# Kernel tuning notes

Measured on AMD Instinct MI355X. Metric: run time of the kernel, lower is better.

Reference implementation:

```python
import jax, jax.numpy as jnp
import numpy as np

N, E, ND, ED, H, OUT, L, VC = 10000, 160000, 8, 4, 128, 256, 6, 6
HEADS, C = 4, 128  # GATConv: out_channels=128 per head, concat=False -> mean over heads


def _ln(x, g, b, eps=1e-5):
    m = x.mean(-1, keepdims=True)
    v = ((x - m) ** 2).mean(-1, keepdims=True)
    return (x - m) * jax.lax.rsqrt(v + eps) * g + b


def _gat_layer(h, src, dst, e_attr, lw, a_src, a_dst, lew, a_edge, bias):
    # h: [N,H]; e_attr: [Etot,H]; PyG GATConv(heads=4, concat=False, edge_dim=H)
    xh = (h @ lw).reshape(N, HEADS, C)                 # [N,4,128]
    eh = (e_attr @ lew).reshape(-1, HEADS, C)          # [Etot,4,128]
    al_s = jnp.einsum('nhc,hc->nh', xh, a_src)
    al_d = jnp.einsum('nhc,hc->nh', xh, a_dst)
    al_e = jnp.einsum('ehc,hc->eh', eh, a_edge)
    alpha = jax.nn.leaky_relu(al_s[src] + al_d[dst] + al_e, 0.2)  # [Etot,4]
    amax = jax.ops.segment_max(alpha, dst, num_segments=N)
    ex = jnp.exp(alpha - amax[dst])
    den = jax.ops.segment_sum(ex, dst, num_segments=N)
    w = ex / (den[dst] + 1e-16)
    out = jax.ops.segment_sum(xh[src] * w[..., None], dst, num_segments=N)  # [N,4,128]
    return out.mean(axis=1) + bias


def setup_inputs() -> dict:
    key = jax.random.key(0)
    ks = jax.random.split(key, 32)
    s = 0.05
    d = {
        'x': jax.random.normal(ks[0], (N, ND), jnp.float32),
        'edge_index': jax.random.randint(ks[1], (2, E), 0, N),
        'edge_attr': jax.random.uniform(ks[2], (E, ED), jnp.float32),
        'vnf_context': jax.random.normal(ks[3], (1, VC), jnp.float32),
        # node embedding
        'node_w': jax.random.normal(ks[4], (ND, H)) * s, 'node_b': jnp.zeros((H,)),
        # EdgeAttentionLayer
        'ea_proj_w': jax.random.normal(ks[5], (ED, H)) * s, 'ea_proj_b': jnp.zeros((H,)),
        'vnf_w': jax.random.normal(ks[6], (VC, H)) * s, 'vnf_b': jnp.zeros((H,)),
        'att1_w': jax.random.normal(ks[7], (2 * H, H)) * s, 'att1_b': jnp.zeros((H,)),
        'att2_w': jax.random.normal(ks[8], (H, H // 2)) * s, 'att2_b': jnp.zeros((H // 2,)),
        'att3_w': jax.random.normal(ks[9], (H // 2, 1)) * s, 'att3_b': jnp.zeros((1,)),
        # per-layer GATConv params (stacked over L layers)
        'gat_lin_w': jax.random.normal(ks[10], (L, H, HEADS * C)) * s,
        'gat_att_src': jax.random.normal(ks[11], (L, HEADS, C)) * s,
        'gat_att_dst': jax.random.normal(ks[12], (L, HEADS, C)) * s,
        'gat_lin_edge_w': jax.random.normal(ks[13], (L, H, HEADS * C)) * s,
        'gat_att_edge': jax.random.normal(ks[14], (L, HEADS, C)) * s,
        'gat_bias': jnp.zeros((L, C)),
        'ln_scale': jnp.ones((L, H)), 'ln_bias': jnp.zeros((L, H)),
        # output projection
        'out_w': jax.random.normal(ks[15], (H, OUT)) * s, 'out_b': jnp.zeros((OUT,)),
    }
    return d


def reference(x, edge_index, edge_attr, vnf_context, node_w, node_b, ea_proj_w, ea_proj_b,
              vnf_w, vnf_b, att1_w, att1_b, att2_w, att2_b, att3_w, att3_b,
              gat_lin_w, gat_att_src, gat_att_dst, gat_lin_edge_w, gat_att_edge, gat_bias,
              ln_scale, ln_bias, out_w, out_b):
    src, dst = edge_index[0], edge_index[1]
    h = x @ node_w + node_b                                   # [N,128]
    # EdgeAttentionLayer (eval mode, no network_state)
    ef = edge_attr @ ea_proj_w + ea_proj_b                    # [E,128]
    vnf = vnf_context @ vnf_w + vnf_b                         # [1,128]
    comb = jnp.concatenate([ef, jnp.broadcast_to(vnf, (E, H))], axis=-1)
    a = jax.nn.relu(comb @ att1_w + att1_b)
    a = jax.nn.relu(a @ att2_w + att2_b)
    e_gate = jax.nn.sigmoid(a @ att3_w + att3_b)              # [E,1]
    w_edge = ef * e_gate                                      # [E,128]
    # GATConv default add_self_loops=True, fill_value='mean'
    loop = jnp.arange(N)
    src2 = jnp.concatenate([src, loop])
    dst2 = jnp.concatenate([dst, loop])
    e2 = jnp.concatenate([w_edge, jnp.broadcast_to(w_edge.mean(0, keepdims=True), (N, H))], axis=0)
    for l in range(L):
        hc = _gat_layer(h, src2, dst2, e2, gat_lin_w[l], gat_att_src[l], gat_att_dst[l],
                        gat_lin_edge_w[l], gat_att_edge[l], gat_bias[l])
        h = _ln(h + jax.nn.relu(hc), ln_scale[l], ln_bias[l])
    return h @ out_w + out_b                                  # [N,256]
```

## Files before the change

### kernel.cpp

```cpp
#include <hip/hip_runtime.h>
#include <hip/hip_bf16.h>
#include <math.h>

#define Nn 10000
#define Ee 160000
#define ET 170000
#define LL 6

typedef short v8s __attribute__((ext_vector_type(8)));
typedef float v4f __attribute__((ext_vector_type(4)));

__device__ __forceinline__ unsigned short f2bf(float v) {
    unsigned int b = __float_as_uint(v);
    b += 0x7fffu + ((b >> 16) & 1u);
    return (unsigned short)(b >> 16);
}
__device__ __forceinline__ float bflo(unsigned int u) { return __uint_as_float(u << 16); }
__device__ __forceinline__ float bfhi(unsigned int u) { return __uint_as_float(u & 0xffff0000u); }

__global__ __launch_bounds__(256) void k_first(
    const float* __restrict__ x, const float* __restrict__ nw,
    const float* __restrict__ nb, float* __restrict__ h, unsigned short* __restrict__ hb,
    const int* __restrict__ ei, int* __restrict__ hist,
    const float* __restrict__ glw, const float* __restrict__ gas,
    const float* __restrict__ gad, const float* __restrict__ glew,
    const float* __restrict__ gae, float* __restrict__ Bs,
    float* __restrict__ Bd, float* __restrict__ Be) {
    int b = blockIdx.x, t = threadIdx.x;
    if (b < 5000) {
        int idx = b * 256 + t;
        int n = idx >> 7, c = idx & 127;
        const float* xr = x + (size_t)n * 8;
        float acc = nb[c];
#pragma unroll
        for (int k = 0; k < 8; k++) acc += xr[k] * nw[k * 128 + c];
        h[idx] = acc;
        hb[idx] = f2bf(acc);
        return;
    }
    if (b < 5665) {
        int i = (b - 5000) * 256 + t;
        if (i < ET) {
            int d = (i < Ee) ? ei[Ee + i] : (i - Ee);
            atomicAdd(&hist[d], 1);
        }
        return;
    }
    {
        int idx = (b - 5665) * 256 + t;
        if (idx >= LL * 128 * 4) return;
        int hh = idx & 3, k = (idx >> 2) & 127, l = idx >> 9;
        const float* lwp = glw  + (size_t)l * 65536 + k * 512 + hh * 128;
        const float* lep = glew + (size_t)l * 65536 + k * 512 + hh * 128;
        const float* sp = gas + l * 512 + hh * 128;
        const float* dp = gad + l * 512 + hh * 128;
        const float* ep = gae + l * 512 + hh * 128;
        float s1 = 0, s2 = 0, s3 = 0;
        for (int c = 0; c < 128; c++) {
            float lv = lwp[c];
            s1 += lv * sp[c];
            s2 += lv * dp[c];
            s3 += lep[c] * ep[c];
        }
        Bs[idx] = s1; Bd[idx] = s2; Be[idx] = s3;
    }
}

__global__ __launch_bounds__(256) void k_setup(
    const float* __restrict__ glw, unsigned short* __restrict__ WsumT,
    const float* __restrict__ a2w, unsigned short* __restrict__ w2bf,
    const float* __restrict__ vnfc, const float* __restrict__ vw,
    const float* __restrict__ vb, const float* __restrict__ eab,
    const float* __restrict__ a1w, const float* __restrict__ a1b,
    const float* __restrict__ eaw, float* __restrict__ E1,
    const float* __restrict__ Be, float* __restrict__ PB, float* __restrict__ cB) {
    __shared__ float vr[128];
    __shared__ float sM1[512];
    __shared__ float sd1[128];
    int b = blockIdx.x, t = threadIdx.x;
    if (b < 1536) {
        int idx = b * 256 + t;
        int kk = idx & 511;
        int c = (idx >> 9) & 127;
        int l = idx >> 16;
        float v = 0.25f * glw[(size_t)l * 65536 + (size_t)(kk & 127) * 512 + (kk >> 7) * 128 + c];
        WsumT[(size_t)l * 65536 + (size_t)c * 512 + kk] = f2bf(v);
        return;
    }
    if (b < 1568) {
        int idx = (b - 1536) * 256 + t;
        int j = idx & 7, lane = (idx >> 3) & 63, nt = (idx >> 9) & 3, ks = idx >> 11;
        int k = ks * 32 + ((lane >> 4) << 3) + j;
        int n = nt * 16 + (lane & 15);
        w2bf[idx] = f2bf(a2w[k * 64 + n]);
        return;
    }
    if (b == 1568) {
        if (t < 128) {
            float a = vb[t];
#pragma unroll
            for (int k = 0; k < 6; k++) a += vnfc[k] * vw[k * 128 + t];
            vr[t] = a;
        }
        __syncthreads();
        if (t < 128) {
            float a = a1b[t];
            for (int k = 0; k < 128; k++) a += eab[k] * a1w[k * 128 + t];
            for (int k = 0; k < 128; k++) a += vr[k] * a1w[(128 + k) * 128 + t];
            sd1[t] = a;
        }
#pragma unroll
        for (int rr = 0; rr < 2; rr++) {
            int id = rr * 256 + t;
            int r = id >> 7, j = id & 127;
            float a = 0.f;
            for (int k = 0; k < 128; k++) a += eaw[r * 128 + k] * a1w[k * 128 + j];
            sM1[id] = a;
        }
        __syncthreads();
        if (t < 128) {
            E1[t * 8 + 0] = sM1[t];
            E1[t * 8 + 1] = sM1[128 + t];
            E1[t * 8 + 2] = sM1[256 + t];
            E1[t * 8 + 3] = sM1[384 + t];
            E1[t * 8 + 4] = sd1[t];
            E1[t * 8 + 5] = 0.f; E1[t * 8 + 6] = 0.f; E1[t * 8 + 7] = 0.f;
        }
        return;
    }
    {
        if (t >= 24) return;
        int l = t >> 2, hh = t & 3;
        const float* bp = Be + l * 512 + hh;
        float s0 = 0, s1 = 0, s2 = 0, s3 = 0, sc = 0;
        for (int k = 0; k < 128; k++) {
            float bv = bp[k * 4];
            s0 += eaw[0 * 128 + k] * bv;
            s1 += eaw[1 * 128 + k] * bv;
            s2 += eaw[2 * 128 + k] * bv;
            s3 += eaw[3 * 128 + k] * bv;
            sc += eab[k] * bv;
        }
        PB[0 * 24 + t] = s0; PB[1 * 24 + t] = s1;
        PB[2 * 24 + t] = s2; PB[3 * 24 + t] = s3;
        cB[t] = sc;
    }
}

__global__ __launch_bounds__(1024) void k_scan(const int* __restrict__ hist,
                                               int* __restrict__ seg, int* __restrict__ pos) {
    __shared__ int wsums[16];
    __shared__ int carry_s;
    int t = threadIdx.x;
    int lane = t & 63, wid = t >> 6;
    if (t == 0) { carry_s = 0; seg[0] = 0; }
    __syncthreads();
    for (int base = 0; base < Nn; base += 1024) {
        int idx = base + t;
        int v = (idx < Nn) ? hist[idx] : 0;
        int sc = v;
#pragma unroll
        for (int d = 1; d < 64; d <<= 1) {
            int up = __shfl_up(sc, d);
            if (lane >= d) sc += up;
        }
        if (lane == 63) wsums[wid] = sc;
        __syncthreads();
        if (wid == 0) {
            int wv = (lane < 16) ? wsums[lane] : 0;
            int wsc = wv;
#pragma unroll
            for (int d = 1; d < 16; d <<= 1) {
                int up = __shfl_up(wsc, d);
                if (lane >= d) wsc += up;
            }
            if (lane < 16) wsums[lane] = wsc - wv;
        }
        __syncthreads();
        int carry = carry_s;
        int inc = sc + wsums[wid] + carry;
        if (idx < Nn) { seg[idx + 1] = inc; pos[idx] = inc - v; }
        __syncthreads();
        if (t == 1023) carry_s = inc;
        __syncthreads();
    }
}

__global__ void k_scatter(const int* __restrict__ ei, int* __restrict__ pos,
                          int* __restrict__ srcv, int* __restrict__ inv,
                          int* __restrict__ loopslot) {
    int i = blockIdx.x * 256 + threadIdx.x;
    if (i >= ET) return;
    int s, d;
    if (i < Ee) { s = ei[i]; d = ei[Ee + i]; } else { s = d = i - Ee; }
    int idx = atomicAdd(&pos[d], 1);
    srcv[idx] = s;
    if (i < Ee) inv[i] = idx;
    else        loopslot[i - Ee] = idx;
}

__global__ __launch_bounds__(256, 2) void k_edge(
    const float* __restrict__ ea, const float* __restrict__ E1,
    const unsigned short* __restrict__ w2bf,
    const float* __restrict__ a2b, const float* __restrict__ a3w,
    const float* __restrict__ a3b,
    const float* __restrict__ PB, const float* __restrict__ cB,
    const int* __restrict__ inv,
    float* __restrict__ aleT, float* __restrict__ gsum) {
    __shared__ float4 sM[128];
    __shared__ float sD[128];
    __shared__ float4 sevs[256];
    __shared__ float gsh[256];
    __shared__ float sgsum[5];
    int t = threadIdx.x;
    int lane = t & 63;
    int wid = t >> 6;
    int c = lane & 15, q = lane >> 4;
    int eb0 = blockIdx.x * 256;

    sevs[t] = *(const float4*)(ea + (size_t)(eb0 + t) * 4);
    if (t < 128) {
        int slot = t ^ ((t >> 3) & 3);
        sM[slot] = *(const float4*)(E1 + t * 8);
        sD[t] = E1[t * 8 + 4];
    }
    if (t < 5) sgsum[t] = 0.f;
    __syncthreads();

    float4 ev4[4];
#pragma unroll
    for (int mt = 0; mt < 4; mt++) ev4[mt] = sevs[(wid * 4 + mt) * 16 + c];

    v8s av[4][4];
#pragma unroll
    for (int ks = 0; ks < 4; ks++) {
        float4 mr[8]; float dr[8];
#pragma unroll
        for (int j = 0; j < 8; j++) {
            int k = ks * 32 + q * 8 + j;
            mr[j] = sM[k ^ q];
            dr[j] = sD[k];
        }
#pragma unroll
        for (int mt = 0; mt < 4; mt++) {
            float4 ev = ev4[mt];
            v8s a;
#pragma unroll
            for (int j = 0; j < 8; j++) {
                float xv = fmaxf(dr[j] + ev.x * mr[j].x + ev.y * mr[j].y
                                       + ev.z * mr[j].z + ev.w * mr[j].w, 0.f);
                a[j] = (short)f2bf(xv);
            }
            av[mt][ks] = a;
        }
    }

    v4f acc[4][4];
#pragma unroll
    for (int nt = 0; nt < 4; nt++) {
        float bb = a2b[nt * 16 + c];
#pragma unroll
        for (int mt = 0; mt < 4; mt++) acc[mt][nt] = (v4f){bb, bb, bb, bb};
    }
#pragma unroll
    for (int nt = 0; nt < 4; nt++) {
#pragma unroll
        for (int ks = 0; ks < 4; ks++) {
            v8s bfr = *(const v8s*)(w2bf + ((size_t)(ks * 4 + nt) * 64 + lane) * 8);
#pragma unroll
            for (int mt = 0; mt < 4; mt++)
                acc[mt][nt] = __builtin_amdgcn_mfma_f32_16x16x32_bf16(av[mt][ks], bfr, acc[mt][nt], 0, 0, 0);
        }
    }

    float a3r[4];
#pragma unroll
    for (int nt = 0; nt < 4; nt++) a3r[nt] = a3w[nt * 16 + c];
    float a3b0 = a3b[0];
#pragma unroll
    for (int mt = 0; mt < 4; mt++) {
#pragma unroll
        for (int r = 0; r < 4; r++) {
            float s = 0.f;
#pragma unroll
            for (int nt = 0; nt < 4; nt++) s += fmaxf(acc[mt][nt][r], 0.f) * a3r[nt];
            s += __shfl_xor(s, 1); s += __shfl_xor(s, 2);
            s += __shfl_xor(s, 4); s += __shfl_xor(s, 8);
            if (c == 0) gsh[(wid * 4 + mt) * 16 + q * 4 + r] = 1.f / (1.f + __expf(-(s + a3b0)));
        }
    }
    __syncthreads();

    float g = gsh[t];
    float4 evv = sevs[t];
    float v0 = g, v1 = g * evv.x, v2 = g * evv.y, v3 = g * evv.z, v4 = g * evv.w;
#pragma unroll
    for (int d = 32; d > 0; d >>= 1) {
        v0 += __shfl_down(v0, d); v1 += __shfl_down(v1, d); v2 += __shfl_down(v2, d);
        v3 += __shfl_down(v3, d); v4 += __shfl_down(v4, d);
    }
    if (lane == 0) {
        atomicAdd(&sgsum[0], v0); atomicAdd(&sgsum[1], v1); atomicAdd(&sgsum[2], v2);
        atomicAdd(&sgsum[3], v3); atomicAdd(&sgsum[4], v4);
    }
    __syncthreads();
    if (t < 5) atomicAdd(&gsum[t], sgsum[t]);
    int slot = inv[eb0 + t];
#pragma unroll
    for (int i4 = 0; i4 < 6; i4++) {
        float4 cc = *(const float4*)(cB + i4 * 4);
        float4 p0 = *(const float4*)(PB + 0 * 24 + i4 * 4);
        float4 p1 = *(const float4*)(PB + 1 * 24 + i4 * 4);
        float4 p2 = *(const float4*)(PB + 2 * 24 + i4 * 4);
        float4 p3 = *(const float4*)(PB + 3 * 24 + i4 * 4);
        float4 o;
        o.x = g * (cc.x + evv.x * p0.x + evv.y * p1.x + evv.z * p2.x + evv.w * p3.x);
        o.y = g * (cc.y + evv.x * p0.y + evv.y * p1.y + evv.z * p2.y + evv.w * p3.y);
        o.z = g * (cc.z + evv.x * p0.z + evv.y * p1.z + evv.z * p2.z + evv.w * p3.z);
        o.w = g * (cc.w + evv.x * p0.w + evv.y * p1.w + evv.z * p2.w + evv.w * p3.w);
        *(float4*)(aleT + (size_t)i4 * ET * 4 + (size_t)slot * 4) = o;
    }
}

__global__ __launch_bounds__(256) void k_abfill(
    const float* __restrict__ h, const float* __restrict__ Bs_l,
    const float* __restrict__ Bd_l, float* __restrict__ als, float* __restrict__ ald,
    const int* __restrict__ loopslot, const float* __restrict__ gsum,
    const float* __restrict__ PB, const float* __restrict__ cB,
    float* __restrict__ aleT) {
    int b = blockIdx.x, t = threadIdx.x;
    if (b < 313) {
        int idx = b * 256 + t;
        if (idx >= Nn * 8) return;
        int n = idx >> 3, slot = idx & 7;
        const float* B = (slot < 4) ? Bs_l : Bd_l;
        int hh = slot & 3;
        const float4* hr = (const float4*)(h + (size_t)n * 128);
        float s = 0.f;
#pragma unroll 8
        for (int kb = 0; kb < 32; kb++) {
            float4 hv = hr[kb];
            s += hv.x * B[(4 * kb + 0) * 4 + hh] + hv.y * B[(4 * kb + 1) * 4 + hh]
               + hv.z * B[(4 * kb + 2) * 4 + hh] + hv.w * B[(4 * kb + 3) * 4 + hh];
        }
        if (slot < 4) als[n * 4 + hh] = s;
        else          ald[n * 4 + hh] = s;
        return;
    }
    {
        int idx = (b - 313) * 256 + t;
        if (idx >= LL * Nn) return;
        int l = idx / Nn;
        int j = idx - l * Nn;
        int slot = loopslot[j];
        float g0 = gsum[0], g1 = gsum[1], g2 = gsum[2], g3 = gsum[3], g4 = gsum[4];
        float4 cc = *(const float4*)(cB + l * 4);
        float4 p0 = *(const float4*)(PB + 0 * 24 + l * 4);
        float4 p1 = *(const float4*)(PB + 1 * 24 + l * 4);
        float4 p2 = *(const float4*)(PB + 2 * 24 + l * 4);
        float4 p3 = *(const float4*)(PB + 3 * 24 + l * 4);
        float4 o;
        o.x = (g0 * cc.x + g1 * p0.x + g2 * p1.x + g3 * p2.x + g4 * p3.x) * (1.0f / Ee);
        o.y = (g0 * cc.y + g1 * p0.y + g2 * p1.y + g3 * p2.y + g4 * p3.y) * (1.0f / Ee);
        o.z = (g0 * cc.z + g1 * p0.z + g2 * p1.z + g3 * p2.z + g4 * p3.z) * (1.0f / Ee);
        o.w = (g0 * cc.w + g1 * p0.w + g2 * p1.w + g3 * p2.w + g4 * p3.w) * (1.0f / Ee);
        *(float4*)(aleT + (size_t)l * ET * 4 + (size_t)slot * 4) = o;
    }
}

__global__ __launch_bounds__(256) void k_agg3(
    const int* __restrict__ srcv, const int* __restrict__ seg,
    const float* __restrict__ als, const float* __restrict__ ald,
    const float* __restrict__ aleS_l,
    const unsigned short* __restrict__ hb, unsigned short* __restrict__ aggb) {
    __shared__ float part[2][512];
    __shared__ float pden[2][4];
    int t = threadIdx.x;
    int lane = t & 63;
    int wv = (t >> 6) & 1;
    int w = t >> 7;
    int n = blockIdx.x * 2 + w;
    int start = seg[n], end = seg[n + 1];
    int deg = end - start;
    int half = (deg + 1) >> 1;
    int s0 = start + wv * half;
    int e0 = wv ? end : start + half;
    int hp = lane >> 4;
    int cch = (lane & 15) * 8;
    float aldh = ald[n * 4 + hp];
    float den = 0.f;
    float4 acc0 = make_float4(0.f, 0.f, 0.f, 0.f);
    float4 acc1 = make_float4(0.f, 0.f, 0.f, 0.f);
    int i = s0;
    for (; i + 2 <= e0; i += 2) {
        int sa = srcv[i], sb = srcv[i + 1];
        float ala = aleS_l[(size_t)i * 4 + hp];
        float alb = aleS_l[(size_t)(i + 1) * 4 + hp];
        float ava = als[sa * 4 + hp] + aldh + ala;
        float avb = als[sb * 4 + hp] + aldh + alb;
        ava = ava > 0.f ? ava : 0.2f * ava;
        avb = avb > 0.f ? avb : 0.2f * avb;
        float ea = __expf(fminf(ava, 60.f));
        float eb = __expf(fminf(avb, 60.f));
        den += ea + eb;
        uint4 ua = *(const uint4*)(hb + (size_t)sa * 128 + cch);
        uint4 ub = *(const uint4*)(hb + (size_t)sb * 128 + cch);
        acc0.x += ea * bflo(ua.x) + eb * bflo(ub.x);
        acc0.y += ea * bfhi(ua.x) + eb * bfhi(ub.x);
        acc0.z += ea * bflo(ua.y) + eb * bflo(ub.y);
        acc0.w += ea * bfhi(ua.y) + eb * bfhi(ub.y);
        acc1.x += ea * bflo(ua.z) + eb * bflo(ub.z);
        acc1.y += ea * bfhi(ua.z) + eb * bfhi(ub.z);
        acc1.z += ea * bflo(ua.w) + eb * bflo(ub.w);
        acc1.w += ea * bfhi(ua.w) + eb * bfhi(ub.w);
    }
    if (i < e0) {
        int sa = srcv[i];
        float ala = aleS_l[(size_t)i * 4 + hp];
        float ava = als[sa * 4 + hp] + aldh + ala;
        ava = ava > 0.f ? ava : 0.2f * ava;
        float ea = __expf(fminf(ava, 60.f));
        den += ea;
        uint4 ua = *(const uint4*)(hb + (size_t)sa * 128 + cch);
        acc0.x += ea * bflo(ua.x); acc0.y += ea * bfhi(ua.x);
        acc0.z += ea * bflo(ua.y); acc0.w += ea * bfhi(ua.y);
        acc1.x += ea * bflo(ua.z); acc1.y += ea * bfhi(ua.z);
        acc1.z += ea * bflo(ua.w); acc1.w += ea * bfhi(ua.w);
    }
    if (wv == 1) {
        *(float4*)&part[w][lane * 8] = acc0;
        *(float4*)&part[w][lane * 8 + 4] = acc1;
        if ((lane & 15) == 0) pden[w][hp] = den;
    }
    __syncthreads();
    if (wv == 0) {
        float4 p0 = *(const float4*)&part[w][lane * 8];
        float4 p1 = *(const float4*)&part[w][lane * 8 + 4];
        float inv2 = 1.f / (den + pden[w][hp] + 1e-16f);
        acc0.x = (acc0.x + p0.x) * inv2; acc0.y = (acc0.y + p0.y) * inv2;
        acc0.z = (acc0.z + p0.z) * inv2; acc0.w = (acc0.w + p0.w) * inv2;
        acc1.x = (acc1.x + p1.x) * inv2; acc1.y = (acc1.y + p1.y) * inv2;
        acc1.z = (acc1.z + p1.z) * inv2; acc1.w = (acc1.w + p1.w) * inv2;
        ushort4 q0, q1;
        q0.x = f2bf(acc0.x); q0.y = f2bf(acc0.y); q0.z = f2bf(acc0.z); q0.w = f2bf(acc0.w);
        q1.x = f2bf(acc1.x); q1.y = f2bf(acc1.y); q1.z = f2bf(acc1.z); q1.w = f2bf(acc1.w);
        *(ushort4*)(aggb + (size_t)n * 512 + lane * 8) = q0;
        *(ushort4*)(aggb + (size_t)n * 512 + lane * 8 + 4) = q1;
    }
}

__global__ __launch_bounds__(256) void k_post(
    const unsigned short* __restrict__ aggb, const unsigned short* __restrict__ WsumT_l,
    const float* __restrict__ gbias, const float* __restrict__ lnsc,
    const float* __restrict__ lnbi, float* __restrict__ h,
    unsigned short* __restrict__ hb, const float* __restrict__ Bs_n,
    const float* __restrict__ Bd_n, float* __restrict__ als, float* __restrict__ ald) {
    int t = threadIdx.x;
    int lane = t & 63, w = t >> 6;
    int n0 = (blockIdx.x * 4 + w) * 16;
    if (n0 >= Nn) return;
    int m = lane & 15, q = lane >> 4;
    v4f acc[8];
#pragma unroll
    for (int nt = 0; nt < 8; nt++) acc[nt] = (v4f){0.f, 0.f, 0.f, 0.f};
    const unsigned short* arow = aggb + (size_t)(n0 + m) * 512 + q * 8;
#pragma unroll 4
    for (int ks = 0; ks < 16; ks++) {
        v8s fa = *(const v8s*)(arow + ks * 32);
#pragma unroll
        for (int nt = 0; nt < 8; nt++) {
            int col = nt * 16 + m;
            v8s fb = *(const v8s*)(WsumT_l + (size_t)col * 512 + ks * 32 + q * 8);
            acc[nt] = __builtin_amdgcn_mfma_f32_16x16x32_bf16(fa, fb, acc[nt], 0, 0, 0);
        }
    }
    float v[8][4];
    float s1[4] = {0.f, 0.f, 0.f, 0.f}, s2[4] = {0.f, 0.f, 0.f, 0.f};
#pragma unroll
    for (int nt = 0; nt < 8; nt++) {
        int col = nt * 16 + m;
        float b = gbias[col];
#pragma unroll
        for (int r = 0; r < 4; r++) {
            int row = n0 + q * 4 + r;
            float val = h[(size_t)row * 128 + col] + fmaxf(acc[nt][r] + b, 0.f);
            v[nt][r] = val;
            s1[r] += val; s2[r] += val * val;
        }
    }
#pragma unroll
    for (int d = 1; d <= 8; d <<= 1) {
#pragma unroll
        for (int r = 0; r < 4; r++) {
            s1[r] += __shfl_xor(s1[r], d);
            s2[r] += __shfl_xor(s2[r], d);
        }
    }
    float o8[8][4];
#pragma unroll
    for (int r = 0; r < 4; r++) {
        float mean = s1[r] * (1.f / 128.f);
        float var = s2[r] * (1.f / 128.f) - mean * mean;
        float rinv = rsqrtf(var + 1e-5f);
        int row = n0 + q * 4 + r;
#pragma unroll
        for (int nt = 0; nt < 8; nt++) {
            int col = nt * 16 + m;
            float o = (v[nt][r] - mean) * rinv * lnsc[col] + lnbi[col];
            o8[nt][r] = o;
            h[(size_t)row * 128 + col] = o;
            hb[(size_t)row * 128 + col] = f2bf(o);
        }
    }
    float sal[4][4], sad[4][4];
#pragma unroll
    for (int r = 0; r < 4; r++) {
#pragma unroll
        for (int hh = 0; hh < 4; hh++) { sal[r][hh] = 0.f; sad[r][hh] = 0.f; }
    }
#pragma unroll
    for (int nt = 0; nt < 8; nt++) {
        int col = nt * 16 + m;
        float4 bs = *(const float4*)(Bs_n + col * 4);
        float4 bd = *(const float4*)(Bd_n + col * 4);
#pragma unroll
        for (int r = 0; r < 4; r++) {
            float o = o8[nt][r];
            sal[r][0] += o * bs.x; sal[r][1] += o * bs.y;
            sal[r][2] += o * bs.z; sal[r][3] += o * bs.w;
            sad[r][0] += o * bd.x; sad[r][1] += o * bd.y;
            sad[r][2] += o * bd.z; sad[r][3] += o * bd.w;
        }
    }
#pragma unroll
    for (int d = 1; d <= 8; d <<= 1) {
#pragma unroll
        for (int r = 0; r < 4; r++) {
#pragma unroll
            for (int hh = 0; hh < 4; hh++) {
                sal[r][hh] += __shfl_xor(sal[r][hh], d);
                sad[r][hh] += __shfl_xor(sad[r][hh], d);
            }
        }
    }
    if (m < 8) {
        int hh = m & 3;
#pragma unroll
        for (int r = 0; r < 4; r++) {
            int row = n0 + q * 4 + r;
            float va = (hh == 0) ? sal[r][0] : (hh == 1) ? sal[r][1] : (hh == 2) ? sal[r][2] : sal[r][3];
            float vd = (hh == 0) ? sad[r][0] : (hh == 1) ? sad[r][1] : (hh == 2) ? sad[r][2] : sad[r][3];
            if (m < 4) als[row * 4 + hh] = va;
            else       ald[row * 4 + hh] = vd;
        }
    }
}

__global__ __launch_bounds__(256) void k_out(
    const float* __restrict__ h, const float* __restrict__ ow,
    const float* __restrict__ ob, float* __restrict__ out) {
    __shared__ float4 hs4[8][32];
    int t = threadIdx.x;
    int n0 = blockIdx.x * 8;
    if (t < 256) {
        int i = t >> 5, kb = t & 31;
        hs4[i][kb] = *(const float4*)(h + (size_t)(n0 + i) * 128 + 4 * kb);
    }
    __syncthreads();
    float acc[8] = {0, 0, 0, 0, 0, 0, 0, 0};
    for (int kb = 0; kb < 32; kb++) {
        float w0 = ow[(4 * kb + 0) * 256 + t];
        float w1 = ow[(4 * kb + 1) * 256 + t];
        float w2 = ow[(4 * kb + 2) * 256 + t];
        float w3 = ow[(4 * kb + 3) * 256 + t];
#pragma unroll
        for (int i = 0; i < 8; i++) {
            float4 hv = hs4[i][kb];
            acc[i] += hv.x * w0 + hv.y * w1 + hv.z * w2 + hv.w * w3;
        }
    }
    float b = ob[t];
#pragma unroll
    for (int i = 0; i < 8; i++) out[(size_t)(n0 + i) * 256 + t] = acc[i] + b;
}

extern "C" void kernel_launch(void* const* d_in, const int* in_sizes, int n_in,
                              void* d_out, int out_size, void* d_ws, size_t ws_size,
                              hipStream_t stream) {
    const float* x    = (const float*)d_in[0];
    const int*   ei   = (const int*)d_in[1];
    const float* ea   = (const float*)d_in[2];
    const float* vnfc = (const float*)d_in[3];
    const float* nw   = (const float*)d_in[4];
    const float* nb   = (const float*)d_in[5];
    const float* eaw  = (const float*)d_in[6];
    const float* eab  = (const float*)d_in[7];
    const float* vw   = (const float*)d_in[8];
    const float* vb   = (const float*)d_in[9];
    const float* a1w  = (const float*)d_in[10];
    const float* a1b  = (const float*)d_in[11];
    const float* a2w  = (const float*)d_in[12];
    const float* a2b  = (const float*)d_in[13];
    const float* a3w  = (const float*)d_in[14];
    const float* a3b  = (const float*)d_in[15];
    const float* glw  = (const float*)d_in[16];
    const float* gas  = (const float*)d_in[17];
    const float* gad  = (const float*)d_in[18];
    const float* glew = (const float*)d_in[19];
    const float* gae  = (const float*)d_in[20];
    const float* gb   = (const float*)d_in[21];
    const float* lnsc = (const float*)d_in[22];
    const float* lnbi = (const float*)d_in[23];
    const float* ow   = (const float*)d_in[24];
    const float* ob   = (const float*)d_in[25];
    float* out = (float*)d_out;

    char* w = (char*)d_ws;
    size_t o = 0;
    auto allocf = [&](size_t cnt) { float* p = (float*)(w + o); o += ((cnt * 4 + 255) / 256) * 256; return p; };
    auto alloci = [&](size_t cnt) { int* p = (int*)(w + o); o += ((cnt * 4 + 255) / 256) * 256; return p; };
    auto allocu = [&](size_t cnt) { unsigned short* p = (unsigned short*)(w + o); o += ((cnt * 2 + 255) / 256) * 256; return p; };
    float* h      = allocf((size_t)Nn * 128);
    unsigned short* hb    = allocu((size_t)Nn * 128);
    unsigned short* aggb  = allocu((size_t)Nn * 512);
    unsigned short* WsumT = allocu((size_t)LL * 128 * 512);
    unsigned short* w2bf  = allocu(8192);
    float* als    = allocf((size_t)Nn * 4);
    float* ald    = allocf((size_t)Nn * 4);
    float* aleT   = allocf((size_t)LL * ET * 4);
    float* Bs     = allocf(3072);
    float* Bd     = allocf(3072);
    float* Be     = allocf(3072);
    float* E1     = allocf(1024);
    float* PB     = allocf(96);
    float* cB     = allocf(24);
    float* gsum   = allocf(8);
    int* seg      = alloci(Nn + 1);
    int* hist     = alloci(Nn);
    int* pos      = alloci(Nn);
    int* srcv     = alloci(ET);
    int* inv      = alloci(Ee);
    int* loopslot = alloci(Nn);

    hipMemsetAsync(hist, 0, Nn * sizeof(int), stream);
    hipMemsetAsync(gsum, 0, 8 * sizeof(float), stream);

    k_first<<<5677, 256, 0, stream>>>(x, nw, nb, h, hb, ei, hist,
                                      glw, gas, gad, glew, gae, Bs, Bd, Be);
    k_setup<<<1570, 256, 0, stream>>>(glw, WsumT, a2w, w2bf, vnfc, vw, vb, eab,
                                      a1w, a1b, eaw, E1, Be, PB, cB);
    k_scan<<<1, 1024, 0, stream>>>(hist, seg, pos);
    k_scatter<<<(ET + 255) / 256, 256, 0, stream>>>(ei, pos, srcv, inv, loopslot);
    k_edge<<<Ee / 256, 256, 0, stream>>>(ea, E1, w2bf, a2b, a3w, a3b, PB, cB, inv, aleT, gsum);
    k_abfill<<<548, 256, 0, stream>>>(h, Bs, Bd, als, ald, loopslot, gsum, PB, cB, aleT);
    for (int l = 0; l < LL; l++) {
        int ln = (l + 1) % LL;
        k_agg3<<<Nn / 2, 256, 0, stream>>>(srcv, seg, als, ald,
                                           aleT + (size_t)l * ET * 4, hb, aggb);
        k_post<<<(625 + 3) / 4, 256, 0, stream>>>(aggb, WsumT + (size_t)l * 65536,
                                                  gb + l * 128, lnsc + l * 128, lnbi + l * 128,
                                                  h, hb, Bs + ln * 512, Bd + ln * 512, als, ald);
    }
    k_out<<<Nn / 8, 256, 0, stream>>>(h, ow, ob, out);
}
```

Measured before the change: 497.8 us.

## Merge setup kernels, fold CSR scatter into edge kernel, unroll aggregation by four

```diff
diff --git a/kernel.cpp b/kernel.cpp
--- a/kernel.cpp
+++ b/kernel.cpp
@@ -25,7 +25,16 @@
     const float* __restrict__ glw, const float* __restrict__ gas,
     const float* __restrict__ gad, const float* __restrict__ glew,
     const float* __restrict__ gae, float* __restrict__ Bs,
-    float* __restrict__ Bd, float* __restrict__ Be) {
+    float* __restrict__ Bd, float* __restrict__ Be,
+    unsigned short* __restrict__ WsumT,
+    const float* __restrict__ a2w, unsigned short* __restrict__ w2bf,
+    const float* __restrict__ vnfc, const float* __restrict__ vw,
+    const float* __restrict__ vb, const float* __restrict__ eab,
+    const float* __restrict__ a1w, const float* __restrict__ a1b,
+    const float* __restrict__ eaw, float* __restrict__ E1) {
+    __shared__ float vr[128];
+    __shared__ float sM1[512];
+    __shared__ float sd1[128];
     int b = blockIdx.x, t = threadIdx.x;
     if (b < 5000) {
         int idx = b * 256 + t;
@@ -46,7 +55,7 @@
         }
         return;
     }
-    {
+    if (b < 5677) {
         int idx = (b - 5665) * 256 + t;
         if (idx >= LL * 128 * 4) return;
         int hh = idx & 3, k = (idx >> 2) & 127, l = idx >> 9;
@@ -63,23 +72,10 @@
             s3 += lep[c] * ep[c];
         }
         Bs[idx] = s1; Bd[idx] = s2; Be[idx] = s3;
-    }
-}
-
-__global__ __launch_bounds__(256) void k_setup(
-    const float* __restrict__ glw, unsigned short* __restrict__ WsumT,
-    const float* __restrict__ a2w, unsigned short* __restrict__ w2bf,
-    const float* __restrict__ vnfc, const float* __restrict__ vw,
-    const float* __restrict__ vb, const float* __restrict__ eab,
-    const float* __restrict__ a1w, const float* __restrict__ a1b,
-    const float* __restrict__ eaw, float* __restrict__ E1,
-    const float* __restrict__ Be, float* __restrict__ PB, float* __restrict__ cB) {
-    __shared__ float vr[128];
-    __shared__ float sM1[512];
-    __shared__ float sd1[128];
-    int b = blockIdx.x, t = threadIdx.x;
-    if (b < 1536) {
-        int idx = b * 256 + t;
+        return;
+    }
+    if (b < 7213) {
+        int idx = (b - 5677) * 256 + t;
         int kk = idx & 511;
         int c = (idx >> 9) & 127;
         int l = idx >> 16;
@@ -87,15 +83,15 @@
         WsumT[(size_t)l * 65536 + (size_t)c * 512 + kk] = f2bf(v);
         return;
     }
-    if (b < 1568) {
-        int idx = (b - 1536) * 256 + t;
+    if (b < 7245) {
+        int idx = (b - 7213) * 256 + t;
         int j = idx & 7, lane = (idx >> 3) & 63, nt = (idx >> 9) & 3, ks = idx >> 11;
         int k = ks * 32 + ((lane >> 4) << 3) + j;
         int n = nt * 16 + (lane & 15);
         w2bf[idx] = f2bf(a2w[k * 64 + n]);
         return;
     }
-    if (b == 1568) {
+    {
         if (t < 128) {
             float a = vb[t];
 #pragma unroll
@@ -126,9 +122,17 @@
             E1[t * 8 + 4] = sd1[t];
             E1[t * 8 + 5] = 0.f; E1[t * 8 + 6] = 0.f; E1[t * 8 + 7] = 0.f;
         }
-        return;
-    }
-    {
+    }
+}
+
+__global__ __launch_bounds__(1024) void k_scan(
+    const int* __restrict__ hist, int* __restrict__ seg, int* __restrict__ pos,
+    const float* __restrict__ eaw, const float* __restrict__ eab,
+    const float* __restrict__ Be, float* __restrict__ PB, float* __restrict__ cB) {
+    __shared__ int wsums[16];
+    __shared__ int carry_s;
+    int t = threadIdx.x;
+    if (blockIdx.x == 1) {
         if (t >= 24) return;
         int l = t >> 2, hh = t & 3;
         const float* bp = Be + l * 512 + hh;
@@ -144,14 +148,8 @@
         PB[0 * 24 + t] = s0; PB[1 * 24 + t] = s1;
         PB[2 * 24 + t] = s2; PB[3 * 24 + t] = s3;
         cB[t] = sc;
-    }
-}
-
-__global__ __launch_bounds__(1024) void k_scan(const int* __restrict__ hist,
-                                               int* __restrict__ seg, int* __restrict__ pos) {
-    __shared__ int wsums[16];
-    __shared__ int carry_s;
-    int t = threadIdx.x;
+        return;
+    }
     int lane = t & 63, wid = t >> 6;
     if (t == 0) { carry_s = 0; seg[0] = 0; }
     __syncthreads();
@@ -186,26 +184,13 @@
     }
 }
 
-__global__ void k_scatter(const int* __restrict__ ei, int* __restrict__ pos,
-                          int* __restrict__ srcv, int* __restrict__ inv,
-                          int* __restrict__ loopslot) {
-    int i = blockIdx.x * 256 + threadIdx.x;
-    if (i >= ET) return;
-    int s, d;
-    if (i < Ee) { s = ei[i]; d = ei[Ee + i]; } else { s = d = i - Ee; }
-    int idx = atomicAdd(&pos[d], 1);
-    srcv[idx] = s;
-    if (i < Ee) inv[i] = idx;
-    else        loopslot[i - Ee] = idx;
-}
-
 __global__ __launch_bounds__(256, 2) void k_edge(
     const float* __restrict__ ea, const float* __restrict__ E1,
     const unsigned short* __restrict__ w2bf,
     const float* __restrict__ a2b, const float* __restrict__ a3w,
     const float* __restrict__ a3b,
     const float* __restrict__ PB, const float* __restrict__ cB,
-    const int* __restrict__ inv,
+    const int* __restrict__ ei, int* __restrict__ pos, int* __restrict__ srcv,
     float* __restrict__ aleT, float* __restrict__ gsum) {
     __shared__ float4 sM[128];
     __shared__ float sD[128];
@@ -218,6 +203,8 @@
     int c = lane & 15, q = lane >> 4;
     int eb0 = blockIdx.x * 256;
 
+    int my_src = ei[eb0 + t];
+    int my_dst = ei[Ee + eb0 + t];
     sevs[t] = *(const float4*)(ea + (size_t)(eb0 + t) * 4);
     if (t < 128) {
         int slot = t ^ ((t >> 3) & 3);
@@ -305,7 +292,8 @@
     }
     __syncthreads();
     if (t < 5) atomicAdd(&gsum[t], sgsum[t]);
-    int slot = inv[eb0 + t];
+    int slot = atomicAdd(&pos[my_dst], 1);
+    srcv[slot] = my_src;
 #pragma unroll
     for (int i4 = 0; i4 < 6; i4++) {
         float4 cc = *(const float4*)(cB + i4 * 4);
@@ -325,7 +313,7 @@
 __global__ __launch_bounds__(256) void k_abfill(
     const float* __restrict__ h, const float* __restrict__ Bs_l,
     const float* __restrict__ Bd_l, float* __restrict__ als, float* __restrict__ ald,
-    const int* __restrict__ loopslot, const float* __restrict__ gsum,
+    int* __restrict__ pos, int* __restrict__ srcv, const float* __restrict__ gsum,
     const float* __restrict__ PB, const float* __restrict__ cB,
     float* __restrict__ aleT) {
     int b = blockIdx.x, t = threadIdx.x;
@@ -348,23 +336,25 @@
         return;
     }
     {
-        int idx = (b - 313) * 256 + t;
-        if (idx >= LL * Nn) return;
-        int l = idx / Nn;
-        int j = idx - l * Nn;
-        int slot = loopslot[j];
+        int j = (b - 313) * 256 + t;
+        if (j >= Nn) return;
+        int slot = atomicAdd(&pos[j], 1);
+        srcv[slot] = j;
         float g0 = gsum[0], g1 = gsum[1], g2 = gsum[2], g3 = gsum[3], g4 = gsum[4];
-        float4 cc = *(const float4*)(cB + l * 4);
-        float4 p0 = *(const float4*)(PB + 0 * 24 + l * 4);
-        float4 p1 = *(const float4*)(PB + 1 * 24 + l * 4);
-        float4 p2 = *(const float4*)(PB + 2 * 24 + l * 4);
-        float4 p3 = *(const float4*)(PB + 3 * 24 + l * 4);
-        float4 o;
-        o.x = (g0 * cc.x + g1 * p0.x + g2 * p1.x + g3 * p2.x + g4 * p3.x) * (1.0f / Ee);
-        o.y = (g0 * cc.y + g1 * p0.y + g2 * p1.y + g3 * p2.y + g4 * p3.y) * (1.0f / Ee);
-        o.z = (g0 * cc.z + g1 * p0.z + g2 * p1.z + g3 * p2.z + g4 * p3.z) * (1.0f / Ee);
-        o.w = (g0 * cc.w + g1 * p0.w + g2 * p1.w + g3 * p2.w + g4 * p3.w) * (1.0f / Ee);
-        *(float4*)(aleT + (size_t)l * ET * 4 + (size_t)slot * 4) = o;
+#pragma unroll
+        for (int l = 0; l < LL; l++) {
+            float4 cc = *(const float4*)(cB + l * 4);
+            float4 p0 = *(const float4*)(PB + 0 * 24 + l * 4);
+            float4 p1 = *(const float4*)(PB + 1 * 24 + l * 4);
+            float4 p2 = *(const float4*)(PB + 2 * 24 + l * 4);
+            float4 p3 = *(const float4*)(PB + 3 * 24 + l * 4);
+            float4 o;
+            o.x = (g0 * cc.x + g1 * p0.x + g2 * p1.x + g3 * p2.x + g4 * p3.x) * (1.0f / Ee);
+            o.y = (g0 * cc.y + g1 * p0.y + g2 * p1.y + g3 * p2.y + g4 * p3.y) * (1.0f / Ee);
+            o.z = (g0 * cc.z + g1 * p0.z + g2 * p1.z + g3 * p2.z + g4 * p3.z) * (1.0f / Ee);
+            o.w = (g0 * cc.w + g1 * p0.w + g2 * p1.w + g3 * p2.w + g4 * p3.w) * (1.0f / Ee);
+            *(float4*)(aleT + (size_t)l * ET * 4 + (size_t)slot * 4) = o;
+        }
     }
 }
 
@@ -392,29 +382,37 @@
     float4 acc0 = make_float4(0.f, 0.f, 0.f, 0.f);
     float4 acc1 = make_float4(0.f, 0.f, 0.f, 0.f);
     int i = s0;
-    for (; i + 2 <= e0; i += 2) {
-        int sa = srcv[i], sb = srcv[i + 1];
-        float ala = aleS_l[(size_t)i * 4 + hp];
+    for (; i + 4 <= e0; i += 4) {
+        int sa = srcv[i], sb = srcv[i + 1], sc = srcv[i + 2], sd = srcv[i + 3];
+        float ala = aleS_l[(size_t)(i + 0) * 4 + hp];
         float alb = aleS_l[(size_t)(i + 1) * 4 + hp];
-        float ava = als[sa * 4 + hp] + aldh + ala;
-        float avb = als[sb * 4 + hp] + aldh + alb;
-        ava = ava > 0.f ? ava : 0.2f * ava;
-        avb = avb > 0.f ? avb : 0.2f * avb;
+        float alc = aleS_l[(size_t)(i + 2) * 4 + hp];
+        float ald_ = aleS_l[(size_t)(i + 3) * 4 + hp];
+        float asa = als[sa * 4 + hp], asb = als[sb * 4 + hp];
+        float asc = als[sc * 4 + hp], asd = als[sd * 4 + hp];
+        uint4 ua = *(const uint4*)(hb + (size_t)sa * 128 + cch);
+        uint4 ub = *(const uint4*)(hb + (size_t)sb * 128 + cch);
+        uint4 uc = *(const uint4*)(hb + (size_t)sc * 128 + cch);
+        uint4 ud = *(const uint4*)(hb + (size_t)sd * 128 + cch);
+        float ava = asa + aldh + ala; ava = ava > 0.f ? ava : 0.2f * ava;
+        float avb = asb + aldh + alb; avb = avb > 0.f ? avb : 0.2f * avb;
+        float avc = asc + aldh + alc; avc = avc > 0.f ? avc : 0.2f * avc;
+        float avd = asd + aldh + ald_; avd = avd > 0.f ? avd : 0.2f * avd;
         float ea = __expf(fminf(ava, 60.f));
         float eb = __expf(fminf(avb, 60.f));
-        den += ea + eb;
-        uint4 ua = *(const uint4*)(hb + (size_t)sa * 128 + cch);
-        uint4 ub = *(const uint4*)(hb + (size_t)sb * 128 + cch);
-        acc0.x += ea * bflo(ua.x) + eb * bflo(ub.x);
-        acc0.y += ea * bfhi(ua.x) + eb * bfhi(ub.x);
-        acc0.z += ea * bflo(ua.y) + eb * bflo(ub.y);
-        acc0.w += ea * bfhi(ua.y) + eb * bfhi(ub.y);
-        acc1.x += ea * bflo(ua.z) + eb * bflo(ub.z);
-        acc1.y += ea * bfhi(ua.z) + eb * bfhi(ub.z);
-        acc1.z += ea * bflo(ua.w) + eb * bflo(ub.w);
-        acc1.w += ea * bfhi(ua.w) + eb * bfhi(ub.w);
-    }
-    if (i < e0) {
+        float ec = __expf(fminf(avc, 60.f));
+        float ed = __expf(fminf(avd, 60.f));
+        den += (ea + eb) + (ec + ed);
+        acc0.x += (ea * bflo(ua.x) + eb * bflo(ub.x)) + (ec * bflo(uc.x) + ed * bflo(ud.x));
+        acc0.y += (ea * bfhi(ua.x) + eb * bfhi(ub.x)) + (ec * bfhi(uc.x) + ed * bfhi(ud.x));
+        acc0.z += (ea * bflo(ua.y) + eb * bflo(ub.y)) + (ec * bflo(uc.y) + ed * bflo(ud.y));
+        acc0.w += (ea * bfhi(ua.y) + eb * bfhi(ub.y)) + (ec * bfhi(uc.y) + ed * bfhi(ud.y));
+        acc1.x += (ea * bflo(ua.z) + eb * bflo(ub.z)) + (ec * bflo(uc.z) + ed * bflo(ud.z));
+        acc1.y += (ea * bfhi(ua.z) + eb * bfhi(ub.z)) + (ec * bfhi(uc.z) + ed * bfhi(ud.z));
+        acc1.z += (ea * bflo(ua.w) + eb * bflo(ub.w)) + (ec * bflo(uc.w) + ed * bflo(ud.w));
+        acc1.w += (ea * bfhi(ua.w) + eb * bfhi(ub.w)) + (ec * bfhi(uc.w) + ed * bfhi(ud.w));
+    }
+    for (; i < e0; i++) {
         int sa = srcv[i];
         float ala = aleS_l[(size_t)i * 4 + hp];
         float ava = als[sa * 4 + hp] + aldh + ala;
@@ -620,6 +618,8 @@
     auto allocf = [&](size_t cnt) { float* p = (float*)(w + o); o += ((cnt * 4 + 255) / 256) * 256; return p; };
     auto alloci = [&](size_t cnt) { int* p = (int*)(w + o); o += ((cnt * 4 + 255) / 256) * 256; return p; };
     auto allocu = [&](size_t cnt) { unsigned short* p = (unsigned short*)(w + o); o += ((cnt * 2 + 255) / 256) * 256; return p; };
+    int* hist     = alloci(Nn);
+    float* gsum   = allocf(8);
     float* h      = allocf((size_t)Nn * 128);
     unsigned short* hb    = allocu((size_t)Nn * 128);
     unsigned short* aggb  = allocu((size_t)Nn * 512);
@@ -634,25 +634,20 @@
     float* E1     = allocf(1024);
     float* PB     = allocf(96);
     float* cB     = allocf(24);
-    float* gsum   = allocf(8);
     int* seg      = alloci(Nn + 1);
-    int* hist     = alloci(Nn);
     int* pos      = alloci(Nn);
     int* srcv     = alloci(ET);
-    int* inv      = alloci(Ee);
-    int* loopslot = alloci(Nn);
-
-    hipMemsetAsync(hist, 0, Nn * sizeof(int), stream);
-    hipMemsetAsync(gsum, 0, 8 * sizeof(float), stream);
-
-    k_first<<<5677, 256, 0, stream>>>(x, nw, nb, h, hb, ei, hist,
-                                      glw, gas, gad, glew, gae, Bs, Bd, Be);
-    k_setup<<<1570, 256, 0, stream>>>(glw, WsumT, a2w, w2bf, vnfc, vw, vb, eab,
-                                      a1w, a1b, eaw, E1, Be, PB, cB);
-    k_scan<<<1, 1024, 0, stream>>>(hist, seg, pos);
-    k_scatter<<<(ET + 255) / 256, 256, 0, stream>>>(ei, pos, srcv, inv, loopslot);
-    k_edge<<<Ee / 256, 256, 0, stream>>>(ea, E1, w2bf, a2b, a3w, a3b, PB, cB, inv, aleT, gsum);
-    k_abfill<<<548, 256, 0, stream>>>(h, Bs, Bd, als, ald, loopslot, gsum, PB, cB, aleT);
+
+    hipMemsetAsync(hist, 0, ((size_t)Nn * 4 + 255) / 256 * 256 + 256, stream);
+
+    k_first<<<7246, 256, 0, stream>>>(x, nw, nb, h, hb, ei, hist,
+                                      glw, gas, gad, glew, gae, Bs, Bd, Be,
+                                      WsumT, a2w, w2bf, vnfc, vw, vb, eab,
+                                      a1w, a1b, eaw, E1);
+    k_scan<<<2, 1024, 0, stream>>>(hist, seg, pos, eaw, eab, Be, PB, cB);
+    k_edge<<<Ee / 256, 256, 0, stream>>>(ea, E1, w2bf, a2b, a3w, a3b, PB, cB,
+                                         ei, pos, srcv, aleT, gsum);
+    k_abfill<<<353, 256, 0, stream>>>(h, Bs, Bd, als, ald, pos, srcv, gsum, PB, cB, aleT);
     for (int l = 0; l < LL; l++) {
         int ln = (l + 1) % LL;
         k_agg3<<<Nn / 2, 256, 0, stream>>>(srcv, seg, als, ald,
```

Measured after the change: 476.1 us. -4.4%, faster.
